# Performance work log

Measured on AMD Instinct MI355X. Metric: run time of the kernel, lower is better.

The kernel has to match this reference:

```python
import jax, jax.numpy as jnp
import numpy as np


def setup_inputs() -> dict:
    key = jax.random.key(0)
    kq, kv, ks = jax.random.split(key, 3)
    B, T, nh, N, D = 4, 2048, 8, 64, 128
    Q = jax.random.normal(kq, (B, T, nh, N), dtype=jnp.float32)
    V = jax.random.normal(kv, (B, T, D), dtype=jnp.float32)
    state = jax.random.normal(ks, (B, nh, N, D), dtype=jnp.float32)
    return {"Q": Q, "V": V, "state": state, "return_new_state": 1}


def reference(Q, V, state, return_new_state):
    # Inter-chunk: read recurrent state.  Q:[B,T,nh,N] x state:[B,nh,N,D] -> [B,T,nh,D]
    output = jnp.einsum('BTnN,BnND->BTnD', Q, state)
    new_state = None
    if return_new_state:
        # Q.flatten(2).mT @ V, unflattened: outer-product accumulation Q^T V
        new_state = state + jnp.einsum('BTnN,BTD->BnND', Q, V)
    T = Q.shape[1]
    if T > 1:
        # Strictly-causal intra-chunk term: tril(QQ^T, -1) @ V
        scores = jnp.tril(jnp.einsum('BTnN,BUnN->BnTU', Q, Q), k=-1)
        output = output + jnp.einsum('BnTU,BUD->BTnD', scores, V)
    return (output, new_state)
```

## Files before the change

### kernel.cpp

```cpp
#include <hip/hip_runtime.h>


using floatx4 = __attribute__((ext_vector_type(4))) float;
using shortx8 = __attribute__((ext_vector_type(8))) short;
using shortx4 = __attribute__((ext_vector_type(4))) short;
using float4v = __attribute__((ext_vector_type(4))) float;

#define MFMA16(a, b, c) __builtin_amdgcn_mfma_f32_16x16x32_bf16((a), (b), (c), 0, 0, 0)

__device__ __forceinline__ unsigned short f2bf(float f) {
  unsigned int u = __builtin_bit_cast(unsigned int, f);
  u += 0x7FFFu + ((u >> 16) & 1u);
  return (unsigned short)(u >> 16);
}
__device__ __forceinline__ float bf2f(unsigned short h) {
  unsigned int u = ((unsigned int)h) << 16;
  return __builtin_bit_cast(float, u);
}

__global__ __launch_bounds__(256) void k_phase1(const float* __restrict__ Q,
                                                const float* __restrict__ V,
                                                float* __restrict__ ws1) {
  __shared__ unsigned short Qs[128 * 66];
  __shared__ unsigned short Vs[128 * 130];

  const int id = blockIdx.x;
  const int n = id & 7, g = (id >> 3) & 15, b = id >> 7;
  const int t0 = g * 128;
  const int tid = threadIdx.x;

  const float* qbase = Q + (((b * 2048 + t0) * 8 + n) * 64);
  const float* vbase = V + ((b * 2048 + t0) * 128);

#pragma unroll
  for (int it = 0; it < 8; ++it) {
    int l = tid + it * 256;
    int t = l >> 4, k4 = (l & 15) * 4;
    float4v q = *(const float4v*)(qbase + t * 512 + k4);
    unsigned int p0 = (unsigned int)f2bf(q.x) | ((unsigned int)f2bf(q.y) << 16);
    unsigned int p1 = (unsigned int)f2bf(q.z) | ((unsigned int)f2bf(q.w) << 16);
    *(unsigned int*)&Qs[t * 66 + k4]     = p0;
    *(unsigned int*)&Qs[t * 66 + k4 + 2] = p1;
  }
#pragma unroll
  for (int it = 0; it < 16; ++it) {
    int l = tid + it * 256;
    int u = l >> 5, d4 = (l & 31) * 4;
    float4v v = *(const float4v*)(vbase + u * 128 + d4);
    unsigned int p0 = (unsigned int)f2bf(v.x) | ((unsigned int)f2bf(v.y) << 16);
    unsigned int p1 = (unsigned int)f2bf(v.z) | ((unsigned int)f2bf(v.w) << 16);
    *(unsigned int*)&Vs[u * 130 + d4]     = p0;
    *(unsigned int*)&Vs[u * 130 + d4 + 2] = p1;
  }
  __syncthreads();

  const int wave = tid >> 6, lane = tid & 63;
  const int col = lane & 15, quad = lane >> 4;

  floatx4 acc[8];
#pragma unroll
  for (int dm = 0; dm < 8; ++dm) acc[dm] = (floatx4){0.f, 0.f, 0.f, 0.f};

#pragma unroll
  for (int s = 0; s < 4; ++s) {
    const int tb = s * 32 + quad * 8;
    shortx8 bq;
    {
      const int i = wave * 16 + col;
#pragma unroll
      for (int j = 0; j < 8; ++j) bq[j] = (short)Qs[(tb + j) * 66 + i];
    }
#pragma unroll
    for (int dm = 0; dm < 8; ++dm) {
      shortx8 av;
      const int d = dm * 16 + col;
#pragma unroll
      for (int j = 0; j < 8; ++j) av[j] = (short)Vs[(tb + j) * 130 + d];
      acc[dm] = MFMA16(av, bq, acc[dm]);
    }
  }

  float* wbase = ws1 + (size_t)((b * 8 + n) * 16 + g) * 8192;
#pragma unroll
  for (int dm = 0; dm < 8; ++dm)
#pragma unroll
    for (int r = 0; r < 4; ++r) {
      int d = dm * 16 + quad * 4 + r;
      int i = wave * 16 + col;
      wbase[d * 64 + i] = acc[dm][r];
    }
}

__global__ __launch_bounds__(256) void k_prefix(const float* __restrict__ state,
                                                const float* __restrict__ ws1,
                                                unsigned short* __restrict__ ws2,
                                                float* __restrict__ new_state) {
  int tid = blockIdx.x * 256 + threadIdx.x;
  int bn = tid >> 13;
  int e = tid & 8191;
  int d = e >> 6, i = e & 63;
  float run = state[(bn * 64 + i) * 128 + d];
  const float* w1 = ws1 + (size_t)bn * 16 * 8192 + e;
  unsigned short* w2 = ws2 + (size_t)bn * 16 * 8192 + e;
#pragma unroll
  for (int g = 0; g < 16; ++g) {
    w2[g * 8192] = f2bf(run);
    run += w1[g * 8192];
  }
  new_state[(bn * 64 + i) * 128 + d] = run;
}

__global__ __launch_bounds__(256) void k_phase2(const float* __restrict__ Q,
                                                const float* __restrict__ V,
                                                const unsigned short* __restrict__ ws2,
                                                float* __restrict__ out) {
  __shared__ unsigned short Qs[64 * 72];
  __shared__ unsigned short Vs[64 * 130];
  __shared__ unsigned short Ss[64 * 72];
  __shared__ unsigned short Pt[128 * 72];

  const int id = blockIdx.x;
  const int n = id & 7, g = (id >> 3) & 15, b = id >> 7;
  const int t0 = g * 128;
  const int tid = threadIdx.x;
  const int wave = tid >> 6, lane = tid & 63;
  const int col = lane & 15, quad = lane >> 4;

  {
    const unsigned short* pb = ws2 + (size_t)((b * 8 + n) * 16 + g) * 8192;
#pragma unroll
    for (int it = 0; it < 8; ++it) {
      int l = tid + it * 256;
      int d = l >> 4, i4 = (l & 15) * 4;
      shortx4 v = *(const shortx4*)(pb + l * 4);
      *(shortx4*)&Pt[d * 72 + i4] = v;
    }
  }

  const float* qbase = Q + (((b * 2048 + t0) * 8 + n) * 64);
  const float* vbase = V + ((b * 2048 + t0) * 128);
  float* obase = out + (((b * 2048 + t0) * 8 + n) * 128);

  for (int c = 0; c < 2; ++c) {
#pragma unroll
    for (int it = 0; it < 4; ++it) {
      int l = tid + it * 256;
      int t = l >> 4, k4 = (l & 15) * 4;
      float4v q = *(const float4v*)(qbase + (c * 64 + t) * 512 + k4);
      unsigned int p0 = (unsigned int)f2bf(q.x) | ((unsigned int)f2bf(q.y) << 16);
      unsigned int p1 = (unsigned int)f2bf(q.z) | ((unsigned int)f2bf(q.w) << 16);
      *(unsigned int*)&Qs[t * 72 + k4]     = p0;
      *(unsigned int*)&Qs[t * 72 + k4 + 2] = p1;
    }
#pragma unroll
    for (int it = 0; it < 8; ++it) {
      int l = tid + it * 256;
      int u = l >> 5, d4 = (l & 31) * 4;
      float4v v = *(const float4v*)(vbase + (c * 64 + u) * 128 + d4);
      unsigned int p0 = (unsigned int)f2bf(v.x) | ((unsigned int)f2bf(v.y) << 16);
      unsigned int p1 = (unsigned int)f2bf(v.z) | ((unsigned int)f2bf(v.w) << 16);
      *(unsigned int*)&Vs[u * 130 + d4]     = p0;
      *(unsigned int*)&Vs[u * 130 + d4 + 2] = p1;
    }
    __syncthreads();

    {
      int job = 0;
      for (int ti = 0; ti < 4; ++ti)
        for (int ui = 0; ui <= (ti | 1); ++ui, ++job) {
          if ((job & 3) != wave) continue;
          if (ui > ti) {
#pragma unroll
            for (int r = 0; r < 4; ++r)
              Ss[(ti * 16 + quad * 4 + r) * 72 + ui * 16 + col] = 0;
          } else {
            floatx4 sc = (floatx4){0.f, 0.f, 0.f, 0.f};
#pragma unroll
            for (int s = 0; s < 2; ++s) {
              shortx8 at = *(const shortx8*)&Qs[(ti * 16 + col) * 72 + s * 32 + quad * 8];
              shortx8 au = *(const shortx8*)&Qs[(ui * 16 + col) * 72 + s * 32 + quad * 8];
              sc = MFMA16(at, au, sc);
            }
#pragma unroll
            for (int r = 0; r < 4; ++r) {
              int t = ti * 16 + quad * 4 + r, u = ui * 16 + col;
              Ss[t * 72 + u] = (u < t) ? f2bf(sc[r]) : (unsigned short)0;
            }
          }
        }
    }
    __syncthreads();

    floatx4 acc[4][2];
#pragma unroll
    for (int ti = 0; ti < 4; ++ti)
#pragma unroll
      for (int dj = 0; dj < 2; ++dj) acc[ti][dj] = (floatx4){0.f, 0.f, 0.f, 0.f};

#pragma unroll
    for (int s = 0; s < 2; ++s) {
      shortx8 bp[2];
#pragma unroll
      for (int dj = 0; dj < 2; ++dj)
        bp[dj] = *(const shortx8*)&Pt[((wave * 2 + dj) * 16 + col) * 72 + s * 32 + quad * 8];
#pragma unroll
      for (int ti = 0; ti < 4; ++ti) {
        shortx8 aq = *(const shortx8*)&Qs[(ti * 16 + col) * 72 + s * 32 + quad * 8];
#pragma unroll
        for (int dj = 0; dj < 2; ++dj) acc[ti][dj] = MFMA16(aq, bp[dj], acc[ti][dj]);
      }
    }
#pragma unroll
    for (int s = 0; s < 2; ++s) {
      shortx8 bv[2];
#pragma unroll
      for (int dj = 0; dj < 2; ++dj) {
        int d = (wave * 2 + dj) * 16 + col;
        int ub = s * 32 + quad * 8;
#pragma unroll
        for (int j = 0; j < 8; ++j) bv[dj][j] = (short)Vs[(ub + j) * 130 + d];
      }
      for (int ti = (s == 0 ? 0 : 2); ti < 4; ++ti) {
        shortx8 as = *(const shortx8*)&Ss[(ti * 16 + col) * 72 + s * 32 + quad * 8];
#pragma unroll
        for (int dj = 0; dj < 2; ++dj) acc[ti][dj] = MFMA16(as, bv[dj], acc[ti][dj]);
      }
    }
#pragma unroll
    for (int ti = 0; ti < 4; ++ti)
#pragma unroll
      for (int dj = 0; dj < 2; ++dj)
#pragma unroll
        for (int r = 0; r < 4; ++r) {
          int t = c * 64 + ti * 16 + quad * 4 + r;
          int d = (wave * 2 + dj) * 16 + col;
          obase[t * 1024 + d] = acc[ti][dj][r];
        }

    if (c == 0) {
      floatx4 ua[8];
#pragma unroll
      for (int dm = 0; dm < 8; ++dm) ua[dm] = (floatx4){0.f, 0.f, 0.f, 0.f};
#pragma unroll
      for (int s = 0; s < 2; ++s) {
        const int tb = s * 32 + quad * 8;
        shortx8 bq;
        {
          const int i = wave * 16 + col;
#pragma unroll
          for (int j = 0; j < 8; ++j) bq[j] = (short)Qs[(tb + j) * 72 + i];
        }
#pragma unroll
        for (int dm = 0; dm < 8; ++dm) {
          shortx8 av;
          const int d = dm * 16 + col;
#pragma unroll
          for (int j = 0; j < 8; ++j) av[j] = (short)Vs[(tb + j) * 130 + d];
          ua[dm] = MFMA16(av, bq, ua[dm]);
        }
      }
      __syncthreads();
#pragma unroll
      for (int dm = 0; dm < 8; ++dm)
#pragma unroll
        for (int r = 0; r < 4; ++r) {
          int d = dm * 16 + quad * 4 + r;
          int i = wave * 16 + col;
          int idx = d * 72 + i;
          Pt[idx] = f2bf(bf2f(Pt[idx]) + ua[dm][r]);
        }
      __syncthreads();
    }
  }
}

extern "C" void kernel_launch(void* const* d_in, const int* in_sizes, int n_in,
                              void* d_out, int out_size, void* d_ws, size_t ws_size,
                              hipStream_t stream) {
  (void)in_sizes; (void)n_in; (void)out_size; (void)ws_size;
  const float* Q     = (const float*)d_in[0];
  const float* V     = (const float*)d_in[1];
  const float* state = (const float*)d_in[2];
  float* out        = (float*)d_out;
  float* new_state  = out + (size_t)4 * 2048 * 8 * 128;
  float* ws1        = (float*)d_ws;
  unsigned short* ws2 = (unsigned short*)((char*)d_ws + (size_t)512 * 8192 * 4);

  k_phase1<<<512, 256, 0, stream>>>(Q, V, ws1);
  k_prefix<<<1024, 256, 0, stream>>>(state, ws1, ws2, new_state);
  k_phase2<<<512, 256, 0, stream>>>(Q, V, ws2, out);
}
```

Before: 115.6 us.

## Transpose Q/V tiles in LDS for vectorized MFMA operand loads and reorder blocks

Stores Q and V transposed in shared memory (k-contiguous) so MFMA operands load as two 64-bit LDS reads instead of eight scalar strided reads. The workspace chunk layout changes to [i][d], which makes the prefix kernel read state and write new_state contiguously. Block ids are remapped so head index is the slowest dimension. The cost is that global loads of Q and V become scalar strided loads during transposition, which may reduce load efficiency.

```diff
diff --git a/kernel.cpp b/kernel.cpp
--- a/kernel.cpp
+++ b/kernel.cpp
@@ -2,9 +2,10 @@
 
 
 using floatx4 = __attribute__((ext_vector_type(4))) float;
+using float4v = __attribute__((ext_vector_type(4))) float;
 using shortx8 = __attribute__((ext_vector_type(8))) short;
 using shortx4 = __attribute__((ext_vector_type(4))) short;
-using float4v = __attribute__((ext_vector_type(4))) float;
+using uint2v  = __attribute__((ext_vector_type(2))) unsigned int;
 
 #define MFMA16(a, b, c) __builtin_amdgcn_mfma_f32_16x16x32_bf16((a), (b), (c), 0, 0, 0)
 
@@ -17,97 +18,100 @@
   unsigned int u = ((unsigned int)h) << 16;
   return __builtin_bit_cast(float, u);
 }
+__device__ __forceinline__ unsigned int pack2(float a, float b) {
+  return (unsigned int)f2bf(a) | ((unsigned int)f2bf(b) << 16);
+}
+__device__ __forceinline__ shortx8 lds8(const unsigned short* p) {
+  shortx4 a = *(const shortx4*)p;
+  shortx4 b = *(const shortx4*)(p + 4);
+  return __builtin_shufflevector(a, b, 0, 1, 2, 3, 4, 5, 6, 7);
+}
 
 __global__ __launch_bounds__(256) void k_phase1(const float* __restrict__ Q,
                                                 const float* __restrict__ V,
                                                 float* __restrict__ ws1) {
-  __shared__ unsigned short Qs[128 * 66];
-  __shared__ unsigned short Vs[128 * 130];
+  __shared__ unsigned short Qt[64 * 132];
+  __shared__ unsigned short Vt[128 * 132];
 
   const int id = blockIdx.x;
-  const int n = id & 7, g = (id >> 3) & 15, b = id >> 7;
+  const int n = id >> 6, bg = id & 63, b = bg >> 4, g = bg & 15;
   const int t0 = g * 128;
   const int tid = threadIdx.x;
 
-  const float* qbase = Q + (((b * 2048 + t0) * 8 + n) * 64);
-  const float* vbase = V + ((b * 2048 + t0) * 128);
-
-#pragma unroll
-  for (int it = 0; it < 8; ++it) {
-    int l = tid + it * 256;
-    int t = l >> 4, k4 = (l & 15) * 4;
-    float4v q = *(const float4v*)(qbase + t * 512 + k4);
-    unsigned int p0 = (unsigned int)f2bf(q.x) | ((unsigned int)f2bf(q.y) << 16);
-    unsigned int p1 = (unsigned int)f2bf(q.z) | ((unsigned int)f2bf(q.w) << 16);
-    *(unsigned int*)&Qs[t * 66 + k4]     = p0;
-    *(unsigned int*)&Qs[t * 66 + k4 + 2] = p1;
-  }
-#pragma unroll
+  const float* qbase = Q + (((size_t)(b * 2048 + t0) * 8 + n) * 64);
+  const float* vbase = V + ((size_t)(b * 2048 + t0) * 128);
+
+#pragma unroll 8
   for (int it = 0; it < 16; ++it) {
-    int l = tid + it * 256;
-    int u = l >> 5, d4 = (l & 31) * 4;
-    float4v v = *(const float4v*)(vbase + u * 128 + d4);
-    unsigned int p0 = (unsigned int)f2bf(v.x) | ((unsigned int)f2bf(v.y) << 16);
-    unsigned int p1 = (unsigned int)f2bf(v.z) | ((unsigned int)f2bf(v.w) << 16);
-    *(unsigned int*)&Vs[u * 130 + d4]     = p0;
-    *(unsigned int*)&Vs[u * 130 + d4 + 2] = p1;
+    int j = tid + it * 256;
+    int i = j & 63, p = j >> 6;
+    float q0 = qbase[(2 * p) * 512 + i];
+    float q1 = qbase[(2 * p + 1) * 512 + i];
+    *(unsigned int*)&Qt[i * 132 + 2 * p] = pack2(q0, q1);
+  }
+#pragma unroll 8
+  for (int it = 0; it < 32; ++it) {
+    int j = tid + it * 256;
+    int d = j & 127, p = j >> 7;
+    float v0 = vbase[(2 * p) * 128 + d];
+    float v1 = vbase[(2 * p + 1) * 128 + d];
+    *(unsigned int*)&Vt[d * 132 + 2 * p] = pack2(v0, v1);
   }
   __syncthreads();
 
   const int wave = tid >> 6, lane = tid & 63;
   const int col = lane & 15, quad = lane >> 4;
 
-  floatx4 acc[8];
-#pragma unroll
-  for (int dm = 0; dm < 8; ++dm) acc[dm] = (floatx4){0.f, 0.f, 0.f, 0.f};
+  floatx4 acc[4][2];
+#pragma unroll
+  for (int ti = 0; ti < 4; ++ti)
+#pragma unroll
+    for (int dj = 0; dj < 2; ++dj) acc[ti][dj] = (floatx4){0.f, 0.f, 0.f, 0.f};
 
 #pragma unroll
   for (int s = 0; s < 4; ++s) {
-    const int tb = s * 32 + quad * 8;
-    shortx8 bq;
-    {
-      const int i = wave * 16 + col;
-#pragma unroll
-      for (int j = 0; j < 8; ++j) bq[j] = (short)Qs[(tb + j) * 66 + i];
-    }
-#pragma unroll
-    for (int dm = 0; dm < 8; ++dm) {
-      shortx8 av;
-      const int d = dm * 16 + col;
-#pragma unroll
-      for (int j = 0; j < 8; ++j) av[j] = (short)Vs[(tb + j) * 130 + d];
-      acc[dm] = MFMA16(av, bq, acc[dm]);
+    const int koff = s * 32 + quad * 8;
+    shortx8 bv[2];
+#pragma unroll
+    for (int dj = 0; dj < 2; ++dj)
+      bv[dj] = lds8(&Vt[((wave * 2 + dj) * 16 + col) * 132 + koff]);
+#pragma unroll
+    for (int ti = 0; ti < 4; ++ti) {
+      shortx8 aq = lds8(&Qt[(ti * 16 + col) * 132 + koff]);
+#pragma unroll
+      for (int dj = 0; dj < 2; ++dj) acc[ti][dj] = MFMA16(aq, bv[dj], acc[ti][dj]);
     }
   }
 
   float* wbase = ws1 + (size_t)((b * 8 + n) * 16 + g) * 8192;
 #pragma unroll
-  for (int dm = 0; dm < 8; ++dm)
-#pragma unroll
-    for (int r = 0; r < 4; ++r) {
-      int d = dm * 16 + quad * 4 + r;
-      int i = wave * 16 + col;
-      wbase[d * 64 + i] = acc[dm][r];
-    }
+  for (int ti = 0; ti < 4; ++ti)
+#pragma unroll
+    for (int dj = 0; dj < 2; ++dj)
+#pragma unroll
+      for (int r = 0; r < 4; ++r) {
+        int i = ti * 16 + quad * 4 + r;
+        int d = (wave * 2 + dj) * 16 + col;
+        wbase[i * 128 + d] = acc[ti][dj][r];
+      }
 }
 
 __global__ __launch_bounds__(256) void k_prefix(const float* __restrict__ state,
                                                 const float* __restrict__ ws1,
                                                 unsigned short* __restrict__ ws2,
                                                 float* __restrict__ new_state) {
-  int tid = blockIdx.x * 256 + threadIdx.x;
-  int bn = tid >> 13;
-  int e = tid & 8191;
-  int d = e >> 6, i = e & 63;
-  float run = state[(bn * 64 + i) * 128 + d];
-  const float* w1 = ws1 + (size_t)bn * 16 * 8192 + e;
-  unsigned short* w2 = ws2 + (size_t)bn * 16 * 8192 + e;
+  int t = blockIdx.x * 256 + threadIdx.x;
+  int bn = t >> 13;
+  int e = t & 8191;
+  float run = state[bn * 8192 + e];
+  const float* w1 = ws1 + (size_t)bn * 131072 + e;
+  unsigned short* w2 = ws2 + (size_t)bn * 131072 + e;
 #pragma unroll
   for (int g = 0; g < 16; ++g) {
     w2[g * 8192] = f2bf(run);
     run += w1[g * 8192];
   }
-  new_state[(bn * 64 + i) * 128 + d] = run;
+  new_state[bn * 8192 + e] = run;
 }
 
 __global__ __launch_bounds__(256) void k_phase2(const float* __restrict__ Q,
@@ -115,52 +119,52 @@
                                                 const unsigned short* __restrict__ ws2,
                                                 float* __restrict__ out) {
   __shared__ unsigned short Qs[64 * 72];
-  __shared__ unsigned short Vs[64 * 130];
+  __shared__ unsigned short Vt[128 * 68];
   __shared__ unsigned short Ss[64 * 72];
-  __shared__ unsigned short Pt[128 * 72];
+  __shared__ unsigned short Pt[128 * 68];
 
   const int id = blockIdx.x;
-  const int n = id & 7, g = (id >> 3) & 15, b = id >> 7;
+  const int n = id >> 6, bg = id & 63, b = bg >> 4, g = bg & 15;
   const int t0 = g * 128;
   const int tid = threadIdx.x;
   const int wave = tid >> 6, lane = tid & 63;
   const int col = lane & 15, quad = lane >> 4;
 
   {
-    const unsigned short* pb = ws2 + (size_t)((b * 8 + n) * 16 + g) * 8192;
-#pragma unroll
-    for (int it = 0; it < 8; ++it) {
-      int l = tid + it * 256;
-      int d = l >> 4, i4 = (l & 15) * 4;
-      shortx4 v = *(const shortx4*)(pb + l * 4);
-      *(shortx4*)&Pt[d * 72 + i4] = v;
-    }
-  }
-
-  const float* qbase = Q + (((b * 2048 + t0) * 8 + n) * 64);
-  const float* vbase = V + ((b * 2048 + t0) * 128);
-  float* obase = out + (((b * 2048 + t0) * 8 + n) * 128);
+    const unsigned int* pb32 =
+        (const unsigned int*)(ws2 + (size_t)((b * 8 + n) * 16 + g) * 8192);
+#pragma unroll 8
+    for (int it = 0; it < 16; ++it) {
+      int j = tid + it * 256;
+      int d2 = j & 63, i = j >> 6;
+      unsigned int u = pb32[i * 64 + d2];
+      Pt[(2 * d2) * 68 + i] = (unsigned short)(u & 0xFFFFu);
+      Pt[(2 * d2 + 1) * 68 + i] = (unsigned short)(u >> 16);
+    }
+  }
+
+  const float* qbase = Q + (((size_t)(b * 2048 + t0) * 8 + n) * 64);
+  const float* vbase = V + ((size_t)(b * 2048 + t0) * 128);
+  float* obase = out + (((size_t)(b * 2048 + t0) * 8 + n) * 128);
 
   for (int c = 0; c < 2; ++c) {
 #pragma unroll
     for (int it = 0; it < 4; ++it) {
       int l = tid + it * 256;
       int t = l >> 4, k4 = (l & 15) * 4;
-      float4v q = *(const float4v*)(qbase + (c * 64 + t) * 512 + k4);
-      unsigned int p0 = (unsigned int)f2bf(q.x) | ((unsigned int)f2bf(q.y) << 16);
-      unsigned int p1 = (unsigned int)f2bf(q.z) | ((unsigned int)f2bf(q.w) << 16);
-      *(unsigned int*)&Qs[t * 72 + k4]     = p0;
-      *(unsigned int*)&Qs[t * 72 + k4 + 2] = p1;
-    }
-#pragma unroll
-    for (int it = 0; it < 8; ++it) {
-      int l = tid + it * 256;
-      int u = l >> 5, d4 = (l & 31) * 4;
-      float4v v = *(const float4v*)(vbase + (c * 64 + u) * 128 + d4);
-      unsigned int p0 = (unsigned int)f2bf(v.x) | ((unsigned int)f2bf(v.y) << 16);
-      unsigned int p1 = (unsigned int)f2bf(v.z) | ((unsigned int)f2bf(v.w) << 16);
-      *(unsigned int*)&Vs[u * 130 + d4]     = p0;
-      *(unsigned int*)&Vs[u * 130 + d4 + 2] = p1;
+      float4v q = *(const float4v*)(qbase + (size_t)(c * 64 + t) * 512 + k4);
+      uint2v u;
+      u.x = pack2(q.x, q.y);
+      u.y = pack2(q.z, q.w);
+      *(uint2v*)&Qs[t * 72 + k4] = u;
+    }
+#pragma unroll 8
+    for (int it = 0; it < 16; ++it) {
+      int j = tid + it * 256;
+      int d = j & 127, p = j >> 7;
+      float v0 = vbase[(size_t)(c * 64 + 2 * p) * 128 + d];
+      float v1 = vbase[(size_t)(c * 64 + 2 * p + 1) * 128 + d];
+      *(unsigned int*)&Vt[d * 68 + 2 * p] = pack2(v0, v1);
     }
     __syncthreads();
 
@@ -199,29 +203,27 @@
 
 #pragma unroll
     for (int s = 0; s < 2; ++s) {
+      const int koff = s * 32 + quad * 8;
       shortx8 bp[2];
 #pragma unroll
       for (int dj = 0; dj < 2; ++dj)
-        bp[dj] = *(const shortx8*)&Pt[((wave * 2 + dj) * 16 + col) * 72 + s * 32 + quad * 8];
+        bp[dj] = lds8(&Pt[((wave * 2 + dj) * 16 + col) * 68 + koff]);
 #pragma unroll
       for (int ti = 0; ti < 4; ++ti) {
-        shortx8 aq = *(const shortx8*)&Qs[(ti * 16 + col) * 72 + s * 32 + quad * 8];
+        shortx8 aq = *(const shortx8*)&Qs[(ti * 16 + col) * 72 + koff];
 #pragma unroll
         for (int dj = 0; dj < 2; ++dj) acc[ti][dj] = MFMA16(aq, bp[dj], acc[ti][dj]);
       }
     }
 #pragma unroll
     for (int s = 0; s < 2; ++s) {
+      const int koff = s * 32 + quad * 8;
       shortx8 bv[2];
 #pragma unroll
-      for (int dj = 0; dj < 2; ++dj) {
-        int d = (wave * 2 + dj) * 16 + col;
-        int ub = s * 32 + quad * 8;
-#pragma unroll
-        for (int j = 0; j < 8; ++j) bv[dj][j] = (short)Vs[(ub + j) * 130 + d];
-      }
+      for (int dj = 0; dj < 2; ++dj)
+        bv[dj] = lds8(&Vt[((wave * 2 + dj) * 16 + col) * 68 + koff]);
       for (int ti = (s == 0 ? 0 : 2); ti < 4; ++ti) {
-        shortx8 as = *(const shortx8*)&Ss[(ti * 16 + col) * 72 + s * 32 + quad * 8];
+        shortx8 as = *(const shortx8*)&Ss[(ti * 16 + col) * 72 + koff];
 #pragma unroll
         for (int dj = 0; dj < 2; ++dj) acc[ti][dj] = MFMA16(as, bv[dj], acc[ti][dj]);
       }
@@ -234,7 +236,7 @@
         for (int r = 0; r < 4; ++r) {
           int t = c * 64 + ti * 16 + quad * 4 + r;
           int d = (wave * 2 + dj) * 16 + col;
-          obase[t * 1024 + d] = acc[ti][dj][r];
+          obase[(size_t)t * 1024 + d] = acc[ti][dj][r];
         }
 
     if (c == 0) {
@@ -243,19 +245,14 @@
       for (int dm = 0; dm < 8; ++dm) ua[dm] = (floatx4){0.f, 0.f, 0.f, 0.f};
 #pragma unroll
       for (int s = 0; s < 2; ++s) {
-        const int tb = s * 32 + quad * 8;
+        const int koff = s * 32 + quad * 8;
         shortx8 bq;
-        {
-          const int i = wave * 16 + col;
-#pragma unroll
-          for (int j = 0; j < 8; ++j) bq[j] = (short)Qs[(tb + j) * 72 + i];
-        }
+#pragma unroll
+        for (int jj = 0; jj < 8; ++jj)
+          bq[jj] = (short)Qs[(koff + jj) * 72 + wave * 16 + col];
 #pragma unroll
         for (int dm = 0; dm < 8; ++dm) {
-          shortx8 av;
-          const int d = dm * 16 + col;
-#pragma unroll
-          for (int j = 0; j < 8; ++j) av[j] = (short)Vs[(tb + j) * 130 + d];
+          shortx8 av = lds8(&Vt[(dm * 16 + col) * 68 + koff]);
           ua[dm] = MFMA16(av, bq, ua[dm]);
         }
       }
@@ -266,7 +263,7 @@
         for (int r = 0; r < 4; ++r) {
           int d = dm * 16 + quad * 4 + r;
           int i = wave * 16 + col;
-          int idx = d * 72 + i;
+          int idx = d * 68 + i;
           Pt[idx] = f2bf(bf2f(Pt[idx]) + ua[dm][r]);
         }
       __syncthreads();
```

After: 101.3 us. 12.3% less time.
